# Optimization experiments

Measured on AMD Instinct MI355X. Metric: run time of the kernel, lower is better.

Reference implementation:

```python
import jax, jax.numpy as jnp
import numpy as np
from jax import lax

BIG = 1e9  # 1D 'infinity' for rows with no background pixel


def _dist1d(m):
    """m: (B,H,W) float {0,1}. Per-row 1D distance along last axis to nearest 0 of m."""
    xs = jnp.moveaxis(m, -1, 0)  # (W,B,H)
    init = jnp.full(m.shape[:-1], BIG, dtype=jnp.float32)

    def step(c, x):
        c = jnp.where(x == 0, 0.0, jnp.minimum(c + 1.0, BIG))
        return c, c

    _, fwd = lax.scan(step, init, xs)
    _, bwd = lax.scan(step, init, xs[::-1])
    g = jnp.minimum(fwd, bwd[::-1])
    return jnp.moveaxis(g, 0, -1)  # (B,H,W)


def _edt(mask_f):
    """Exact Euclidean distance transform (scipy distance_transform_edt semantics):
    distance from each pixel to the nearest zero of mask_f. mask_f: (B,H,W) float {0,1}."""
    g = _dist1d(mask_f)          # 1D distances along rows
    g2 = g * g                   # (B,H,W)
    H = mask_f.shape[1]
    i = jnp.arange(H, dtype=jnp.float32)
    offs = (i[:, None] - i[None, :]) ** 2  # (H,H)

    def per_sample(g2s):  # (H,W) -> (H,W)
        # d2[i,j] = min_k g2[k,j] + (i-k)^2 ; intermediate (H,H,W)
        return jnp.min(g2s[None, :, :] + offs[:, :, None], axis=1)

    d2 = lax.map(per_sample, g2)
    return jnp.sqrt(d2)


def setup_inputs() -> dict:
    key = jax.random.key(0)
    k1, k2, k3 = jax.random.split(key, 3)
    B, C, H, W = 16, 2, 256, 256
    inputs = jax.random.normal(k1, (B, C, H, W), dtype=jnp.float32)
    targets = jax.random.randint(k2, (B, H, W), 0, 2)
    starget = jax.random.uniform(k3, (B, H, W), dtype=jnp.float32)
    return {"inputs": inputs, "targets": targets, "starget": starget,
            "dice_co": 1, "boundary_co": 1}


def reference(inputs, targets, starget, dice_co, boundary_co):
    f32 = jnp.float32
    tgt_i = targets.astype(jnp.int32)

    # ---- CrossEntropyLoss2d: NLL of log_softmax, mean over all pixels ----
    logp = jax.nn.log_softmax(inputs, axis=1)
    ce = -jnp.mean(jnp.take_along_axis(logp, tgt_i[:, None, :, :], axis=1))

    # ---- DiceLoss: hard-thresholded class-1 prob vs targets, global dice ----
    probs = jax.nn.softmax(inputs, axis=1)
    hard = (probs[:, 1] >= 0.5).astype(f32)
    tflat = targets.astype(f32)
    smooth = 1.0
    dice_coef = (2.0 * jnp.sum(hard * tflat) + smooth) / (jnp.sum(hard) + jnp.sum(tflat) + smooth)
    dice_loss = 1.0 - dice_coef

    # ---- Boundary_Loss: signed EDT of argmax prediction, dot with target one-hot (class 1) ----
    pred = jnp.argmax(inputs, axis=1)           # (B,H,W) int
    pos = (pred == 1).astype(f32)
    neg = 1.0 - pos
    dn = _edt(neg)                              # distance(negmask)
    dp = _edt(pos)                              # distance(posmask)
    res = dn * neg - (dp - 1.0) * pos           # signed distance map, class 1
    has_pos = jnp.any(pos > 0, axis=(1, 2))[:, None, None]
    res = jnp.where(has_pos, res, 0.0)
    t1 = (targets == 1).astype(f32)
    per_sample = jnp.mean(t1 * res, axis=(1, 2))  # SurfaceLoss mean over (1,1,H,W)
    lb = jnp.sum(per_sample)
    boundary = lb * lb                          # module returns loss * loss

    return ce + dice_loss + boundary
```

## Files before the change

### kernel.cpp

```cpp
#include <hip/hip_runtime.h>

#define NB 16
#define HH 256
#define WW 256
#define HWSZ (HH * WW)
#define NPIX (NB * HWSZ)
#define ROWS (NB * HH)

#define OFF_P NPIX
#define OFF_PART2 (NPIX + 5 * ROWS)

#define LOG2E 1.44269504088896340736f
#define LN2 0.69314718055994530942f

__device__ __forceinline__ float softplus_fast(float z) {
  const float u = __builtin_amdgcn_exp2f(-fabsf(z) * LOG2E);
  return fmaxf(z, 0.0f) + LN2 * __builtin_amdgcn_logf(1.0f + u);
}

__global__ __launch_bounds__(256) void stage1_kernel(
    const float* __restrict__ inp, const int* __restrict__ tgt,
    unsigned int* __restrict__ wsu, float* __restrict__ wsf) {
  const int row = blockIdx.x;
  const int b = row >> 8;
  const int i = row & 255;
  const int j = threadIdx.x;

  const size_t base = (size_t)(2 * b) * HWSZ + (size_t)i * WW + j;
  const float x0 = inp[base];
  const float x1 = inp[base + HWSZ];
  const int t = tgt[(size_t)row * WW + j];

  const bool pos = x1 > x0;
  const bool hard = x1 >= x0;

  const float d = x1 - x0;
  const float ce = softplus_fast((t == 1) ? -d : d);

  __shared__ unsigned long long wsh[4];
  const unsigned long long bal = __ballot(pos);
  if ((threadIdx.x & 63) == 0) wsh[threadIdx.x >> 6] = bal;
  __syncthreads();
  unsigned long long wp[4], wn[4];
#pragma unroll
  for (int q = 0; q < 4; ++q) { wp[q] = wsh[q]; wn[q] = ~wsh[q]; }

  const int qj = j >> 6, rj = j & 63;
  const unsigned long long lowmask = (~0ull) >> (63 - rj);
  const unsigned long long himask = (~0ull) << rj;

  int loP = -(1 << 20), loN = -(1 << 20);
#pragma unroll
  for (int q = 0; q < 4; ++q) {
    unsigned long long mp = wp[q], mn = wn[q];
    if (q == qj) { mp &= lowmask; mn &= lowmask; }
    else if (q > qj) { mp = 0ull; mn = 0ull; }
    if (mp) loP = (q << 6) + 63 - __builtin_clzll(mp);
    if (mn) loN = (q << 6) + 63 - __builtin_clzll(mn);
  }
  int hiP = (1 << 20), hiN = (1 << 20);
#pragma unroll
  for (int q = 3; q >= 0; --q) {
    unsigned long long mp = wp[q], mn = wn[q];
    if (q == qj) { mp &= himask; mn &= himask; }
    else if (q < qj) { mp = 0ull; mn = 0ull; }
    if (mp) hiP = (q << 6) + (int)__builtin_ctzll(mp);
    if (mn) hiN = (q << 6) + (int)__builtin_ctzll(mn);
  }
  const int dN = min(j - loP, hiP - j);
  const int dP = min(j - loN, hiN - j);
  const unsigned int dNc = (dN > 255) ? 0xFFFFu : (unsigned int)dN;
  const unsigned int dPc = (dP > 255) ? 0xFFFFu : (unsigned int)dP;
  wsu[(size_t)row * WW + j] = dNc | (dPc << 16);

  const int tf = (t == 1) ? 1 : 0;
  float v0 = ce;
  int p1 = (hard ? 1 : 0) | ((hard && tf) ? 0x10000 : 0);
  int p2 = tf | (pos ? 0x10000 : 0);
#pragma unroll
  for (int off = 32; off > 0; off >>= 1) {
    v0 += __shfl_down(v0, off);
    p1 += __shfl_down(p1, off);
    p2 += __shfl_down(p2, off);
  }
  __shared__ float redf[4];
  __shared__ int redi[4][2];
  const int lane = threadIdx.x & 63, wid = threadIdx.x >> 6;
  if (lane == 0) { redf[wid] = v0; redi[wid][0] = p1; redi[wid][1] = p2; }
  __syncthreads();
  if (threadIdx.x == 0) {
    float sce = 0.f;
    int s1 = 0, s2 = 0;
#pragma unroll
    for (int q = 0; q < 4; ++q) { sce += redf[q]; s1 += redi[q][0]; s2 += redi[q][1]; }
    wsf[OFF_P + 0 * ROWS + row] = sce;
    wsf[OFF_P + 1 * ROWS + row] = (float)(s1 & 0xFFFF);
    wsf[OFF_P + 2 * ROWS + row] = (float)(s1 >> 16);
    wsf[OFF_P + 3 * ROWS + row] = (float)(s2 & 0xFFFF);
    wsf[OFF_P + 4 * ROWS + row] = (float)(s2 >> 16);
  }
}

__global__ __launch_bounds__(256) void stage2_kernel(
    const int* __restrict__ tgt,
    const unsigned int* __restrict__ wsu, float* __restrict__ wsf) {
  const int row = blockIdx.x;
  const int b = row >> 8;
  const int i = row & 255;
  const int j = threadIdx.x;
  const unsigned int* g = wsu + (size_t)b * HWSZ;

  const unsigned int v0 = g[i * WW + j];
  const bool pos = (v0 & 0xFFFFu) == 0u;
  const float a0 = (float)(v0 & 0xFFFFu);
  const float b0 = (float)(v0 >> 16);
  float mN = a0 * a0;
  float mP = b0 * b0;

  const int rmax = max(i, 255 - i);
  for (int r = 1; r <= rmax; ++r) {
    const float rr = (float)(r * r);
    if (!__ballot((rr < mN) || (rr < mP))) break;
    if (i - r >= 0) {
      const unsigned int u = g[(i - r) * WW + j];
      const float a = (float)(u & 0xFFFFu);
      const float bb = (float)(u >> 16);
      mN = fminf(mN, a * a + rr);
      mP = fminf(mP, bb * bb + rr);
    }
    if (i + r < HH) {
      const unsigned int u = g[(i + r) * WW + j];
      const float a = (float)(u & 0xFFFFu);
      const float bb = (float)(u >> 16);
      mN = fminf(mN, a * a + rr);
      mP = fminf(mP, bb * bb + rr);
    }
  }

  const int t = tgt[(size_t)row * WW + j];
  const float res = pos ? (1.0f - sqrtf(mP)) : sqrtf(mN);
  float local = (t == 1) ? res : 0.0f;

#pragma unroll
  for (int off = 32; off > 0; off >>= 1) local += __shfl_down(local, off);
  __shared__ float red[4];
  const int lane = threadIdx.x & 63, wid = threadIdx.x >> 6;
  if (lane == 0) red[wid] = local;
  __syncthreads();
  if (threadIdx.x == 0)
    wsf[OFF_PART2 + row] = red[0] + red[1] + red[2] + red[3];
}

__global__ __launch_bounds__(256) void stage3_kernel(
    const float* __restrict__ wsf, float* __restrict__ out) {
  const int t = threadIdx.x;
  const float* P = wsf + OFF_P;

  float s0 = 0.f, s1 = 0.f, s2 = 0.f, s3 = 0.f;
#pragma unroll
  for (int gi = 0; gi < 16; ++gi) {
    const int idx = t + (gi << 8);
    s0 += P[0 * ROWS + idx];
    s1 += P[1 * ROWS + idx];
    s2 += P[2 * ROWS + idx];
    s3 += P[3 * ROWS + idx];
  }
#pragma unroll
  for (int off = 32; off > 0; off >>= 1) {
    s0 += __shfl_down(s0, off);
    s1 += __shfl_down(s1, off);
    s2 += __shfl_down(s2, off);
    s3 += __shfl_down(s3, off);
  }
  __shared__ float red[4][4];
  const int lane = t & 63, wid = t >> 6;
  if (lane == 0) { red[wid][0] = s0; red[wid][1] = s1; red[wid][2] = s2; red[wid][3] = s3; }

  const int b = t >> 4, m = t & 15;
  float pc = 0.f, sb = 0.f;
#pragma unroll
  for (int k = 0; k < 16; ++k) {
    const int idx = (b << 8) + m + (k << 4);
    pc += P[4 * ROWS + idx];
    sb += wsf[OFF_PART2 + idx];
  }
  pc += __shfl_xor(pc, 1); pc += __shfl_xor(pc, 2);
  pc += __shfl_xor(pc, 4); pc += __shfl_xor(pc, 8);
  sb += __shfl_xor(sb, 1); sb += __shfl_xor(sb, 2);
  sb += __shfl_xor(sb, 4); sb += __shfl_xor(sb, 8);
  __shared__ float pcL[16], sbL[16];
  if (m == 0) { pcL[b] = pc; sbL[b] = sb; }
  __syncthreads();

  if (t == 0) {
    const float ceS = red[0][0] + red[1][0] + red[2][0] + red[3][0];
    const float hS  = red[0][1] + red[1][1] + red[2][1] + red[3][1];
    const float htS = red[0][2] + red[1][2] + red[2][2] + red[3][2];
    const float tS  = red[0][3] + red[1][3] + red[2][3] + red[3][3];
    const float ce = ceS * (1.0f / (float)NPIX);
    const float dice_loss = 1.0f - (2.0f * htS + 1.0f) / (hS + tS + 1.0f);
    float lb = 0.0f;
    for (int bb = 0; bb < NB; ++bb)
      lb += (pcL[bb] > 0.0f) ? sbL[bb] * (1.0f / (float)HWSZ) : 0.0f;
    out[0] = ce + dice_loss + lb * lb;
  }
}

extern "C" void kernel_launch(void* const* d_in, const int* in_sizes, int n_in,
                              void* d_out, int out_size, void* d_ws, size_t ws_size,
                              hipStream_t stream) {
  (void)in_sizes; (void)n_in; (void)out_size; (void)ws_size;
  const float* inp = (const float*)d_in[0];
  const int* tgt = (const int*)d_in[1];
  unsigned int* wsu = (unsigned int*)d_ws;
  float* wsf = (float*)d_ws;
  float* out = (float*)d_out;

  stage1_kernel<<<ROWS, 256, 0, stream>>>(inp, tgt, wsu, wsf);
  stage2_kernel<<<ROWS, 256, 0, stream>>>(tgt, wsu, wsf);
  stage3_kernel<<<1, 256, 0, stream>>>(wsf, out);
}
```

Baseline: 85.61 us.

## Fuse three stages into one cooperative kernel with grid sync and last-block reduction

Replaces the three kernel launches with a single cooperative kernel of 1024 blocks, each handling four rows. The row-wise 1D distance pass and the column-wise EDT search are separated by a grid-wide barrier, and the final reduction runs in whichever block takes the last atomic ticket. This removes two launch gaps and the separate single-block reduction kernel. In exchange it depends on all 1024 blocks being co-resident and pays for a grid sync, with the old three-kernel path kept as a fallback if the cooperative launch fails.

```diff
diff --git a/kernel.cpp b/kernel.cpp
--- a/kernel.cpp
+++ b/kernel.cpp
@@ -1,4 +1,7 @@
 #include <hip/hip_runtime.h>
+#include <hip/hip_cooperative_groups.h>
+
+namespace cg = cooperative_groups;
 
 #define NB 16
 #define HH 256
@@ -7,7 +10,12 @@
 #define NPIX (NB * HWSZ)
 #define ROWS (NB * HH)
 
+#define NBLK 1024
+#define RPB 4
 #define OFF_P NPIX
+#define OFF_TICKET (NPIX + 6 * NBLK)
+
+#define OFF_PL NPIX
 #define OFF_PART2 (NPIX + 5 * ROWS)
 
 #define LOG2E 1.44269504088896340736f
@@ -16,6 +24,213 @@
 __device__ __forceinline__ float softplus_fast(float z) {
   const float u = __builtin_amdgcn_exp2f(-fabsf(z) * LOG2E);
   return fmaxf(z, 0.0f) + LN2 * __builtin_amdgcn_logf(1.0f + u);
+}
+
+__global__ __launch_bounds__(256, 4) void fused_kernel(
+    const float* __restrict__ inp, const int* __restrict__ tgt,
+    unsigned int* __restrict__ wsu, float* __restrict__ wsf,
+    float* __restrict__ out) {
+  const int blk = blockIdx.x;
+  const int r0 = blk * RPB;
+  const int b = r0 >> 8;
+  const int i0 = r0 & 255;
+  const int j = threadIdx.x;
+  const int lane = j & 63, wid = j >> 6;
+
+  if (blk == 0 && j == 0) wsu[OFF_TICKET] = 0u;
+
+  float x0[RPB], x1[RPB];
+  int tt[RPB];
+  const size_t base0 = (size_t)(2 * b) * HWSZ + (size_t)i0 * WW + j;
+#pragma unroll
+  for (int rr = 0; rr < RPB; ++rr) {
+    x0[rr] = inp[base0 + (size_t)rr * WW];
+    x1[rr] = inp[base0 + (size_t)rr * WW + HWSZ];
+    tt[rr] = tgt[(size_t)(r0 + rr) * WW + j];
+  }
+
+  float ceAcc = 0.0f;
+  int p1 = 0, p2 = 0;
+  bool posv[RPB], tb[RPB];
+#pragma unroll
+  for (int rr = 0; rr < RPB; ++rr) {
+    const float d = x1[rr] - x0[rr];
+    const bool pos = x1[rr] > x0[rr];
+    const bool hard = x1[rr] >= x0[rr];
+    const bool tf = (tt[rr] == 1);
+    ceAcc += softplus_fast(tf ? -d : d);
+    p1 += (hard ? 1 : 0) | ((hard && tf) ? 0x10000 : 0);
+    p2 += (tf ? 1 : 0) | (pos ? 0x10000 : 0);
+    posv[rr] = pos;
+    tb[rr] = tf;
+  }
+
+  __shared__ unsigned long long wsh[RPB][4];
+#pragma unroll
+  for (int rr = 0; rr < RPB; ++rr) {
+    const unsigned long long bal = __ballot(posv[rr]);
+    if (lane == 0) wsh[rr][wid] = bal;
+  }
+  __syncthreads();
+
+  const int qj = j >> 6, rj = j & 63;
+  const unsigned long long lowmask = (~0ull) >> (63 - rj);
+  const unsigned long long himask = (~0ull) << rj;
+
+  float mN[RPB], mP[RPB];
+#pragma unroll
+  for (int rr = 0; rr < RPB; ++rr) {
+    unsigned long long wp[4], wn[4];
+#pragma unroll
+    for (int q = 0; q < 4; ++q) { wp[q] = wsh[rr][q]; wn[q] = ~wp[q]; }
+
+    int loP = -(1 << 20), loN = -(1 << 20);
+#pragma unroll
+    for (int q = 0; q < 4; ++q) {
+      unsigned long long mp = wp[q], mn = wn[q];
+      if (q == qj) { mp &= lowmask; mn &= lowmask; }
+      else if (q > qj) { mp = 0ull; mn = 0ull; }
+      if (mp) loP = (q << 6) + 63 - __builtin_clzll(mp);
+      if (mn) loN = (q << 6) + 63 - __builtin_clzll(mn);
+    }
+    int hiP = (1 << 20), hiN = (1 << 20);
+#pragma unroll
+    for (int q = 3; q >= 0; --q) {
+      unsigned long long mp = wp[q], mn = wn[q];
+      if (q == qj) { mp &= himask; mn &= himask; }
+      else if (q < qj) { mp = 0ull; mn = 0ull; }
+      if (mp) hiP = (q << 6) + (int)__builtin_ctzll(mp);
+      if (mn) hiN = (q << 6) + (int)__builtin_ctzll(mn);
+    }
+    const int dN = min(j - loP, hiP - j);
+    const int dP = min(j - loN, hiN - j);
+    const unsigned int dNc = (dN > 255) ? 0xFFFFu : (unsigned int)dN;
+    const unsigned int dPc = (dP > 255) ? 0xFFFFu : (unsigned int)dP;
+    wsu[(size_t)(r0 + rr) * WW + j] = dNc | (dPc << 16);
+    const float aN = (float)dNc, aP = (float)dPc;
+    mN[rr] = aN * aN;
+    mP[rr] = aP * aP;
+  }
+
+  cg::this_grid().sync();
+
+  const unsigned int* g = wsu + (size_t)b * HWSZ;
+  const int rmax = max(i0 + RPB - 1, 255 - i0);
+  for (int r = 1; r <= rmax; ++r) {
+    const float rr2 = (float)(r * r);
+    bool any = false;
+#pragma unroll
+    for (int rr = 0; rr < RPB; ++rr)
+      any = any || (rr2 < mN[rr]) || (rr2 < mP[rr]);
+    if (!__ballot(any)) break;
+#pragma unroll
+    for (int rr = 0; rr < RPB; ++rr) {
+      const int i = i0 + rr;
+      if (i - r >= 0) {
+        const unsigned int u = g[(size_t)(i - r) * WW + j];
+        const float a = (float)(u & 0xFFFFu), bb = (float)(u >> 16);
+        mN[rr] = fminf(mN[rr], a * a + rr2);
+        mP[rr] = fminf(mP[rr], bb * bb + rr2);
+      }
+      if (i + r < HH) {
+        const unsigned int u = g[(size_t)(i + r) * WW + j];
+        const float a = (float)(u & 0xFFFFu), bb = (float)(u >> 16);
+        mN[rr] = fminf(mN[rr], a * a + rr2);
+        mP[rr] = fminf(mP[rr], bb * bb + rr2);
+      }
+    }
+  }
+
+  float bnd = 0.0f;
+#pragma unroll
+  for (int rr = 0; rr < RPB; ++rr) {
+    const float res = posv[rr] ? (1.0f - sqrtf(mP[rr])) : sqrtf(mN[rr]);
+    if (tb[rr]) bnd += res;
+  }
+
+#pragma unroll
+  for (int off = 32; off > 0; off >>= 1) {
+    ceAcc += __shfl_down(ceAcc, off);
+    bnd += __shfl_down(bnd, off);
+    p1 += __shfl_down(p1, off);
+    p2 += __shfl_down(p2, off);
+  }
+  __shared__ float rf[4][2];
+  __shared__ int ri[4][2];
+  if (lane == 0) { rf[wid][0] = ceAcc; rf[wid][1] = bnd; ri[wid][0] = p1; ri[wid][1] = p2; }
+  __syncthreads();
+  if (j == 0) {
+    float sce = 0.f, sbn = 0.f;
+    int s1 = 0, s2 = 0;
+#pragma unroll
+    for (int q = 0; q < 4; ++q) { sce += rf[q][0]; sbn += rf[q][1]; s1 += ri[q][0]; s2 += ri[q][1]; }
+    float* P = wsf + OFF_P;
+    P[0 * NBLK + blk] = sce;
+    P[1 * NBLK + blk] = (float)(s1 & 0xFFFF);
+    P[2 * NBLK + blk] = (float)(s1 >> 16);
+    P[3 * NBLK + blk] = (float)(s2 & 0xFFFF);
+    P[4 * NBLK + blk] = (float)(s2 >> 16);
+    P[5 * NBLK + blk] = sbn;
+  }
+
+  __shared__ int lastFlag;
+  if (j == 0) {
+    __threadfence();
+    const unsigned int old = atomicAdd(wsu + OFF_TICKET, 1u);
+    lastFlag = (old == NBLK - 1) ? 1 : 0;
+  }
+  __syncthreads();
+  if (!lastFlag) return;
+  __threadfence();
+
+  const float* P = wsf + OFF_P;
+  float s0 = 0.f, s1f = 0.f, s2f = 0.f, s3f = 0.f;
+#pragma unroll
+  for (int k = 0; k < 4; ++k) {
+    const int idx = j + (k << 8);
+    s0 += P[0 * NBLK + idx];
+    s1f += P[1 * NBLK + idx];
+    s2f += P[2 * NBLK + idx];
+    s3f += P[3 * NBLK + idx];
+  }
+#pragma unroll
+  for (int off = 32; off > 0; off >>= 1) {
+    s0 += __shfl_down(s0, off);
+    s1f += __shfl_down(s1f, off);
+    s2f += __shfl_down(s2f, off);
+    s3f += __shfl_down(s3f, off);
+  }
+  __shared__ float red[4][4];
+  if (lane == 0) { red[wid][0] = s0; red[wid][1] = s1f; red[wid][2] = s2f; red[wid][3] = s3f; }
+
+  const int bs = j >> 4, m = j & 15;
+  float pc = 0.f, sb = 0.f;
+#pragma unroll
+  for (int k = 0; k < 4; ++k) {
+    const int idx = (bs << 6) + m + (k << 4);
+    pc += P[4 * NBLK + idx];
+    sb += P[5 * NBLK + idx];
+  }
+  pc += __shfl_xor(pc, 1); pc += __shfl_xor(pc, 2);
+  pc += __shfl_xor(pc, 4); pc += __shfl_xor(pc, 8);
+  sb += __shfl_xor(sb, 1); sb += __shfl_xor(sb, 2);
+  sb += __shfl_xor(sb, 4); sb += __shfl_xor(sb, 8);
+  __shared__ float pcL[16], sbL[16];
+  if (m == 0) { pcL[bs] = pc; sbL[bs] = sb; }
+  __syncthreads();
+
+  if (j == 0) {
+    const float ceS = red[0][0] + red[1][0] + red[2][0] + red[3][0];
+    const float hS  = red[0][1] + red[1][1] + red[2][1] + red[3][1];
+    const float htS = red[0][2] + red[1][2] + red[2][2] + red[3][2];
+    const float tS  = red[0][3] + red[1][3] + red[2][3] + red[3][3];
+    const float ce = ceS * (1.0f / (float)NPIX);
+    const float dice_loss = 1.0f - (2.0f * htS + 1.0f) / (hS + tS + 1.0f);
+    float lb = 0.0f;
+    for (int bb = 0; bb < NB; ++bb)
+      lb += (pcL[bb] > 0.0f) ? sbL[bb] * (1.0f / (float)HWSZ) : 0.0f;
+    out[0] = ce + dice_loss + lb * lb;
+  }
 }
 
 __global__ __launch_bounds__(256) void stage1_kernel(
@@ -93,11 +308,11 @@
     int s1 = 0, s2 = 0;
 #pragma unroll
     for (int q = 0; q < 4; ++q) { sce += redf[q]; s1 += redi[q][0]; s2 += redi[q][1]; }
-    wsf[OFF_P + 0 * ROWS + row] = sce;
-    wsf[OFF_P + 1 * ROWS + row] = (float)(s1 & 0xFFFF);
-    wsf[OFF_P + 2 * ROWS + row] = (float)(s1 >> 16);
-    wsf[OFF_P + 3 * ROWS + row] = (float)(s2 & 0xFFFF);
-    wsf[OFF_P + 4 * ROWS + row] = (float)(s2 >> 16);
+    wsf[OFF_PL + 0 * ROWS + row] = sce;
+    wsf[OFF_PL + 1 * ROWS + row] = (float)(s1 & 0xFFFF);
+    wsf[OFF_PL + 2 * ROWS + row] = (float)(s1 >> 16);
+    wsf[OFF_PL + 3 * ROWS + row] = (float)(s2 & 0xFFFF);
+    wsf[OFF_PL + 4 * ROWS + row] = (float)(s2 >> 16);
   }
 }
 
@@ -154,7 +369,7 @@
 __global__ __launch_bounds__(256) void stage3_kernel(
     const float* __restrict__ wsf, float* __restrict__ out) {
   const int t = threadIdx.x;
-  const float* P = wsf + OFF_P;
+  const float* P = wsf + OFF_PL;
 
   float s0 = 0.f, s1 = 0.f, s2 = 0.f, s3 = 0.f;
 #pragma unroll
@@ -216,7 +431,12 @@
   float* wsf = (float*)d_ws;
   float* out = (float*)d_out;
 
-  stage1_kernel<<<ROWS, 256, 0, stream>>>(inp, tgt, wsu, wsf);
-  stage2_kernel<<<ROWS, 256, 0, stream>>>(tgt, wsu, wsf);
-  stage3_kernel<<<1, 256, 0, stream>>>(wsf, out);
-}
+  void* kargs[] = {(void*)&inp, (void*)&tgt, (void*)&wsu, (void*)&wsf, (void*)&out};
+  hipError_t err = hipLaunchCooperativeKernel(
+      (const void*)fused_kernel, dim3(NBLK), dim3(256), kargs, 0, stream);
+  if (err != hipSuccess) {
+    stage1_kernel<<<ROWS, 256, 0, stream>>>(inp, tgt, wsu, wsf);
+    stage2_kernel<<<ROWS, 256, 0, stream>>>(tgt, wsu, wsf);
+    stage3_kernel<<<1, 256, 0, stream>>>(wsf, out);
+  }
+}
```

After: 170.5 us. 1.99x slower.

## Fuse final reduction into stage2 via ticket, one row per wave in stage1

Applied to the files above, without the earlier changes.

Stage1 now processes one row per wavefront, with four elements per lane, so the row-wide ballot and reduction need no shared memory or block barriers. Stage3 is removed: the last stage2 block to finish, detected through an atomic ticket counter in the workspace, performs the final reduction, saving a kernel launch. Stage2 also prefetches the four nearest vertical neighbours before its search loop to overlap their loads. The change adds an atomic and fences per block and relies on stage1 resetting the ticket before stage2 runs.

```diff
diff --git a/kernel.cpp b/kernel.cpp
--- a/kernel.cpp
+++ b/kernel.cpp
@@ -9,6 +9,7 @@
 
 #define OFF_P NPIX
 #define OFF_PART2 (NPIX + 5 * ROWS)
+#define OFF_TICKET (NPIX + 6 * ROWS)
 
 #define LOG2E 1.44269504088896340736f
 #define LN2 0.69314718055994530942f
@@ -21,89 +22,92 @@
 __global__ __launch_bounds__(256) void stage1_kernel(
     const float* __restrict__ inp, const int* __restrict__ tgt,
     unsigned int* __restrict__ wsu, float* __restrict__ wsf) {
-  const int row = blockIdx.x;
+  const int wid = threadIdx.x >> 6;
+  const int lane = threadIdx.x & 63;
+  const int row = (blockIdx.x << 2) + wid;
   const int b = row >> 8;
   const int i = row & 255;
-  const int j = threadIdx.x;
-
-  const size_t base = (size_t)(2 * b) * HWSZ + (size_t)i * WW + j;
-  const float x0 = inp[base];
-  const float x1 = inp[base + HWSZ];
-  const int t = tgt[(size_t)row * WW + j];
-
-  const bool pos = x1 > x0;
-  const bool hard = x1 >= x0;
-
-  const float d = x1 - x0;
-  const float ce = softplus_fast((t == 1) ? -d : d);
-
-  __shared__ unsigned long long wsh[4];
-  const unsigned long long bal = __ballot(pos);
-  if ((threadIdx.x & 63) == 0) wsh[threadIdx.x >> 6] = bal;
-  __syncthreads();
+
+  if (blockIdx.x == 0 && threadIdx.x == 0) wsu[OFF_TICKET] = 0u;
+
+  const size_t ibase = (size_t)(2 * b) * HWSZ + (size_t)i * WW;
+  const size_t tbase = (size_t)row * WW;
+
+  float x0[4], x1[4];
+  int t[4];
+#pragma unroll
+  for (int q = 0; q < 4; ++q) {
+    const int p = (q << 6) + lane;
+    x0[q] = inp[ibase + p];
+    x1[q] = inp[ibase + HWSZ + p];
+    t[q] = tgt[tbase + p];
+  }
+
   unsigned long long wp[4], wn[4];
-#pragma unroll
-  for (int q = 0; q < 4; ++q) { wp[q] = wsh[q]; wn[q] = ~wsh[q]; }
-
-  const int qj = j >> 6, rj = j & 63;
-  const unsigned long long lowmask = (~0ull) >> (63 - rj);
-  const unsigned long long himask = (~0ull) << rj;
-
-  int loP = -(1 << 20), loN = -(1 << 20);
+  float ceAcc = 0.0f;
+  int p1 = 0, p2 = 0;
 #pragma unroll
   for (int q = 0; q < 4; ++q) {
-    unsigned long long mp = wp[q], mn = wn[q];
-    if (q == qj) { mp &= lowmask; mn &= lowmask; }
-    else if (q > qj) { mp = 0ull; mn = 0ull; }
-    if (mp) loP = (q << 6) + 63 - __builtin_clzll(mp);
-    if (mn) loN = (q << 6) + 63 - __builtin_clzll(mn);
-  }
-  int hiP = (1 << 20), hiN = (1 << 20);
-#pragma unroll
-  for (int q = 3; q >= 0; --q) {
-    unsigned long long mp = wp[q], mn = wn[q];
-    if (q == qj) { mp &= himask; mn &= himask; }
-    else if (q < qj) { mp = 0ull; mn = 0ull; }
-    if (mp) hiP = (q << 6) + (int)__builtin_ctzll(mp);
-    if (mn) hiN = (q << 6) + (int)__builtin_ctzll(mn);
-  }
-  const int dN = min(j - loP, hiP - j);
-  const int dP = min(j - loN, hiN - j);
-  const unsigned int dNc = (dN > 255) ? 0xFFFFu : (unsigned int)dN;
-  const unsigned int dPc = (dP > 255) ? 0xFFFFu : (unsigned int)dP;
-  wsu[(size_t)row * WW + j] = dNc | (dPc << 16);
-
-  const int tf = (t == 1) ? 1 : 0;
-  float v0 = ce;
-  int p1 = (hard ? 1 : 0) | ((hard && tf) ? 0x10000 : 0);
-  int p2 = tf | (pos ? 0x10000 : 0);
+    const bool pos = x1[q] > x0[q];
+    const bool hard = x1[q] >= x0[q];
+    const bool tf = (t[q] == 1);
+    const float d = x1[q] - x0[q];
+    ceAcc += softplus_fast(tf ? -d : d);
+    p1 += (hard ? 1 : 0) | ((hard && tf) ? 0x10000 : 0);
+    p2 += (tf ? 1 : 0) | (pos ? 0x10000 : 0);
+    wp[q] = __ballot(pos);
+    wn[q] = ~wp[q];
+  }
+
+  const unsigned long long lowmask = (~0ull) >> (63 - lane);
+  const unsigned long long himask = (~0ull) << lane;
+#pragma unroll
+  for (int q = 0; q < 4; ++q) {
+    int loP = -(1 << 20), loN = -(1 << 20);
+#pragma unroll
+    for (int u = 0; u < 4; ++u) {
+      unsigned long long mp = wp[u], mn = wn[u];
+      if (u == q) { mp &= lowmask; mn &= lowmask; }
+      else if (u > q) { mp = 0ull; mn = 0ull; }
+      if (mp) loP = (u << 6) + 63 - __builtin_clzll(mp);
+      if (mn) loN = (u << 6) + 63 - __builtin_clzll(mn);
+    }
+    int hiP = (1 << 20), hiN = (1 << 20);
+#pragma unroll
+    for (int u = 3; u >= 0; --u) {
+      unsigned long long mp = wp[u], mn = wn[u];
+      if (u == q) { mp &= himask; mn &= himask; }
+      else if (u < q) { mp = 0ull; mn = 0ull; }
+      if (mp) hiP = (u << 6) + (int)__builtin_ctzll(mp);
+      if (mn) hiN = (u << 6) + (int)__builtin_ctzll(mn);
+    }
+    const int p = (q << 6) + lane;
+    const int dN = min(p - loP, hiP - p);
+    const int dP = min(p - loN, hiN - p);
+    const unsigned int dNc = (dN > 255) ? 0xFFFFu : (unsigned int)dN;
+    const unsigned int dPc = (dP > 255) ? 0xFFFFu : (unsigned int)dP;
+    wsu[tbase + p] = dNc | (dPc << 16);
+  }
+
 #pragma unroll
   for (int off = 32; off > 0; off >>= 1) {
-    v0 += __shfl_down(v0, off);
+    ceAcc += __shfl_down(ceAcc, off);
     p1 += __shfl_down(p1, off);
     p2 += __shfl_down(p2, off);
   }
-  __shared__ float redf[4];
-  __shared__ int redi[4][2];
-  const int lane = threadIdx.x & 63, wid = threadIdx.x >> 6;
-  if (lane == 0) { redf[wid] = v0; redi[wid][0] = p1; redi[wid][1] = p2; }
-  __syncthreads();
-  if (threadIdx.x == 0) {
-    float sce = 0.f;
-    int s1 = 0, s2 = 0;
-#pragma unroll
-    for (int q = 0; q < 4; ++q) { sce += redf[q]; s1 += redi[q][0]; s2 += redi[q][1]; }
-    wsf[OFF_P + 0 * ROWS + row] = sce;
-    wsf[OFF_P + 1 * ROWS + row] = (float)(s1 & 0xFFFF);
-    wsf[OFF_P + 2 * ROWS + row] = (float)(s1 >> 16);
-    wsf[OFF_P + 3 * ROWS + row] = (float)(s2 & 0xFFFF);
-    wsf[OFF_P + 4 * ROWS + row] = (float)(s2 >> 16);
+  if (lane == 0) {
+    wsf[OFF_P + 0 * ROWS + row] = ceAcc;
+    wsf[OFF_P + 1 * ROWS + row] = (float)(p1 & 0xFFFF);
+    wsf[OFF_P + 2 * ROWS + row] = (float)(p1 >> 16);
+    wsf[OFF_P + 3 * ROWS + row] = (float)(p2 & 0xFFFF);
+    wsf[OFF_P + 4 * ROWS + row] = (float)(p2 >> 16);
   }
 }
 
 __global__ __launch_bounds__(256) void stage2_kernel(
     const int* __restrict__ tgt,
-    const unsigned int* __restrict__ wsu, float* __restrict__ wsf) {
+    unsigned int* __restrict__ wsu, float* __restrict__ wsf,
+    float* __restrict__ out) {
   const int row = blockIdx.x;
   const int b = row >> 8;
   const int i = row & 255;
@@ -111,14 +115,32 @@
   const unsigned int* g = wsu + (size_t)b * HWSZ;
 
   const unsigned int v0 = g[i * WW + j];
+  unsigned int uA = 0xFFFFFFFFu, uB = 0xFFFFFFFFu, uC = 0xFFFFFFFFu, uD = 0xFFFFFFFFu;
+  if (i - 1 >= 0) uA = g[(i - 1) * WW + j];
+  if (i + 1 < HH) uB = g[(i + 1) * WW + j];
+  if (i - 2 >= 0) uC = g[(i - 2) * WW + j];
+  if (i + 2 < HH) uD = g[(i + 2) * WW + j];
+
   const bool pos = (v0 & 0xFFFFu) == 0u;
   const float a0 = (float)(v0 & 0xFFFFu);
   const float b0 = (float)(v0 >> 16);
   float mN = a0 * a0;
   float mP = b0 * b0;
 
+  {
+    float a, bb;
+    a = (float)(uA & 0xFFFFu); bb = (float)(uA >> 16);
+    mN = fminf(mN, a * a + 1.0f); mP = fminf(mP, bb * bb + 1.0f);
+    a = (float)(uB & 0xFFFFu); bb = (float)(uB >> 16);
+    mN = fminf(mN, a * a + 1.0f); mP = fminf(mP, bb * bb + 1.0f);
+    a = (float)(uC & 0xFFFFu); bb = (float)(uC >> 16);
+    mN = fminf(mN, a * a + 4.0f); mP = fminf(mP, bb * bb + 4.0f);
+    a = (float)(uD & 0xFFFFu); bb = (float)(uD >> 16);
+    mN = fminf(mN, a * a + 4.0f); mP = fminf(mP, bb * bb + 4.0f);
+  }
+
   const int rmax = max(i, 255 - i);
-  for (int r = 1; r <= rmax; ++r) {
+  for (int r = 3; r <= rmax; ++r) {
     const float rr = (float)(r * r);
     if (!__ballot((rr < mN) || (rr < mP))) break;
     if (i - r >= 0) {
@@ -143,23 +165,29 @@
 
 #pragma unroll
   for (int off = 32; off > 0; off >>= 1) local += __shfl_down(local, off);
-  __shared__ float red[4];
+  __shared__ float red2[4];
   const int lane = threadIdx.x & 63, wid = threadIdx.x >> 6;
-  if (lane == 0) red[wid] = local;
+  if (lane == 0) red2[wid] = local;
   __syncthreads();
-  if (threadIdx.x == 0)
-    wsf[OFF_PART2 + row] = red[0] + red[1] + red[2] + red[3];
-}
-
-__global__ __launch_bounds__(256) void stage3_kernel(
-    const float* __restrict__ wsf, float* __restrict__ out) {
-  const int t = threadIdx.x;
+
+  __shared__ int lastFlag;
+  if (threadIdx.x == 0) {
+    wsf[OFF_PART2 + row] = red2[0] + red2[1] + red2[2] + red2[3];
+    __threadfence();
+    const unsigned int old = atomicAdd(wsu + OFF_TICKET, 1u);
+    lastFlag = (old == ROWS - 1) ? 1 : 0;
+  }
+  __syncthreads();
+  if (!lastFlag) return;
+  __threadfence();
+
   const float* P = wsf + OFF_P;
+  const int tt = threadIdx.x;
 
   float s0 = 0.f, s1 = 0.f, s2 = 0.f, s3 = 0.f;
 #pragma unroll
   for (int gi = 0; gi < 16; ++gi) {
-    const int idx = t + (gi << 8);
+    const int idx = tt + (gi << 8);
     s0 += P[0 * ROWS + idx];
     s1 += P[1 * ROWS + idx];
     s2 += P[2 * ROWS + idx];
@@ -173,14 +201,13 @@
     s3 += __shfl_down(s3, off);
   }
   __shared__ float red[4][4];
-  const int lane = t & 63, wid = t >> 6;
   if (lane == 0) { red[wid][0] = s0; red[wid][1] = s1; red[wid][2] = s2; red[wid][3] = s3; }
 
-  const int b = t >> 4, m = t & 15;
+  const int bs = tt >> 4, m = tt & 15;
   float pc = 0.f, sb = 0.f;
 #pragma unroll
   for (int k = 0; k < 16; ++k) {
-    const int idx = (b << 8) + m + (k << 4);
+    const int idx = (bs << 8) + m + (k << 4);
     pc += P[4 * ROWS + idx];
     sb += wsf[OFF_PART2 + idx];
   }
@@ -189,10 +216,10 @@
   sb += __shfl_xor(sb, 1); sb += __shfl_xor(sb, 2);
   sb += __shfl_xor(sb, 4); sb += __shfl_xor(sb, 8);
   __shared__ float pcL[16], sbL[16];
-  if (m == 0) { pcL[b] = pc; sbL[b] = sb; }
+  if (m == 0) { pcL[bs] = pc; sbL[bs] = sb; }
   __syncthreads();
 
-  if (t == 0) {
+  if (tt == 0) {
     const float ceS = red[0][0] + red[1][0] + red[2][0] + red[3][0];
     const float hS  = red[0][1] + red[1][1] + red[2][1] + red[3][1];
     const float htS = red[0][2] + red[1][2] + red[2][2] + red[3][2];
@@ -216,7 +243,6 @@
   float* wsf = (float*)d_ws;
   float* out = (float*)d_out;
 
-  stage1_kernel<<<ROWS, 256, 0, stream>>>(inp, tgt, wsu, wsf);
-  stage2_kernel<<<ROWS, 256, 0, stream>>>(tgt, wsu, wsf);
-  stage3_kernel<<<1, 256, 0, stream>>>(wsf, out);
-}
+  stage1_kernel<<<ROWS / 4, 256, 0, stream>>>(inp, tgt, wsu, wsf);
+  stage2_kernel<<<ROWS, 256, 0, stream>>>(tgt, wsu, wsf, out);
+}
```

After: 161.4 us. 1.89x slower.
